# Performance work log

Hardware: AMD Instinct MI355X
Metric: run time of the kernel (lower is better)

The kernel has to match this reference:

```python
import jax, jax.numpy as jnp
import numpy as np
from jax.ops import segment_sum, segment_max

LRELU = 0.01  # torch F.leaky_relu default negative_slope


def _seg_softmax(e, seg, n):
    # torch_geometric.utils.softmax: stable segment softmax with 1e-16 eps
    m = segment_max(e, seg, num_segments=n)
    ex = jnp.exp(e - m[seg])
    s = segment_sum(ex, seg, num_segments=n)
    return ex / (s[seg] + 1e-16)


def _gcn(x, ei, w):
    j, i = ei[0], ei[1]  # code unpacks (edge_index_j, edge_index_i)
    n = x.shape[0]
    deg = segment_sum(jnp.ones_like(x[:, 0])[i], i, num_segments=n)
    dis = jnp.where(deg > 0, deg ** -0.5, 0.0)
    norm = dis[j] * dis[i]
    agg = segment_sum(norm[:, None] * x[j], i, num_segments=n)  # out[i] += norm*x[j]
    return jax.nn.relu(agg) @ w


def _highway(x1, x2, w, b):
    gate = jax.nn.sigmoid(x1 @ w + b)
    return gate * x2 + (1.0 - gate) * x1


def _gat_r(x, ei, a_i, a_j):
    j, i = ei[0], ei[1]
    n = x.shape[0]
    si = x @ a_i  # [R]
    sj = x @ a_j
    e = si[i] + sj[j]
    alpha = _seg_softmax(jax.nn.leaky_relu(e, LRELU).astype(jnp.float32), j, n)  # grouped by j!
    return jax.nn.relu(segment_sum(alpha[:, None] * x[j], i, num_segments=n))


def _graphattention_wjq(x, ei, rel_all, rel_emb, ww1):
    i, j = ei[0], ei[1]  # this module unpacks (i, j)
    n = x.shape[0]
    ef = jax.nn.leaky_relu(x, LRELU)
    re = jax.nn.leaky_relu(rel_emb, LRELU)
    feat = jnp.concatenate([ef[i], re[rel_all], ef[j]], axis=1)  # [E, 700]
    att = _seg_softmax(feat @ ww1, i, n)
    return segment_sum(feat * att[:, None], i, num_segments=n)  # [N, 700]


def _gat(x, r, ei, rel, a_i, a_j, a_r):
    j, i = ei[0], ei[1]
    n = x.shape[0]
    e = (x @ a_i)[i] + (x @ a_j)[j] + (r @ a_r)[rel]
    alpha = _seg_softmax(jax.nn.leaky_relu(e, LRELU).astype(jnp.float32), i, n)
    return jax.nn.relu(segment_sum(alpha[:, None] * x[j], i, num_segments=n))


def setup_inputs() -> dict:
    key = jax.random.key(0)
    ks = jax.random.split(key, 24)
    N, E, R, ELG, EH, RH = 20000, 150000, 1000, 15000, 300, 100

    def edges(k, n_nodes, n_edges):
        k1, k2 = jax.random.split(k)
        src = jax.random.randint(k1, (n_edges,), 0, n_nodes)
        dst = jax.random.randint(k2, (n_edges,), 0, n_nodes)
        src = jnp.where(src == dst, (src + 1) % n_nodes, src)  # no self-loops
        ring = jnp.arange(n_nodes)  # guarantee in-degree >= 1 everywhere
        src = src.at[:n_nodes].set((ring + 1) % n_nodes)
        dst = dst.at[:n_nodes].set(ring)
        return jnp.stack([src, dst])  # row0 = j (source), row1 = i (target)

    rel = jax.random.randint(ks[3], (E,), 0, R).at[0].set(R - 1)  # branch -> rel_emb1
    p = lambda k, sh: (jax.random.normal(k, sh, jnp.float32) * 0.05)
    return {
        "x_e": jax.random.normal(ks[0], (N, EH), jnp.float32),
        "edge_index": edges(ks[1], N, E),
        "rel": rel,
        "edge_index_all": edges(ks[2], N, E),
        "rel_all": jax.random.randint(ks[4], (E,), 0, 2 * R),
        "line_graph_index_out": edges(ks[5], R, ELG),
        "line_graph_val_out": jax.random.normal(ks[6], (ELG,), jnp.float32),
        "line_graph_index_in": edges(ks[7], R, ELG),
        "line_graph_val_in": jax.random.normal(ks[8], (ELG,), jnp.float32),
        "gcn1_w": p(ks[9], (EH, EH)),
        "gcn2_w": p(ks[10], (EH, EH)),
        "hw1_w": p(ks[11], (EH, EH)),
        "hw1_b": jnp.zeros((EH,), jnp.float32),
        "hw2_w": p(ks[12], (EH, EH)),
        "hw2_b": jnp.zeros((EH,), jnp.float32),
        "ww1": p(ks[13], (2 * EH + RH,)),
        "gat_ai": p(ks[14], (2 * (2 * EH + RH) - 400 + 0,)) if False else p(ks[14], (1000,)),
        "gat_aj": p(ks[15], (1000,)),
        "gat_ar": p(ks[16], (RH,)),
        "gatr_ai": p(ks[17], (RH,)),
        "gatr_aj": p(ks[18], (RH,)),
        "rel_emb1": p(ks[19], (R, RH)),
        "rel_emb2": p(ks[20], (R, RH)),
    }


def reference(x_e, edge_index, rel, edge_index_all, rel_all,
              line_graph_index_out, line_graph_val_out,
              line_graph_index_in, line_graph_val_in,
              gcn1_w, gcn2_w, hw1_w, hw1_b, hw2_w, hw2_b, ww1,
              gat_ai, gat_aj, gat_ar, gatr_ai, gatr_aj, rel_emb1, rel_emb2):
    # RAGA.forward; inputs constructed so rel.max()+1 == rel_emb1.shape[0]
    # (branch taken) and edge_index_all has no self-loops (remove_self_loops no-op).
    x = _highway(x_e, _gcn(x_e, edge_index_all, gcn1_w), hw1_w, hw1_b)
    x = _highway(x, _gcn(x, edge_index_all, gcn2_w), hw2_w, hw2_b)
    rel_emb_out = _gat_r(rel_emb1, line_graph_index_out, gatr_ai, gatr_aj)
    rel_emb_in = _gat_r(rel_emb1, line_graph_index_in, gatr_ai, gatr_aj)
    rel_emb = jnp.concatenate([rel_emb_out, rel_emb_in], axis=0)  # [2R, 100]
    x_wjq = jnp.concatenate(
        [x, _graphattention_wjq(x, edge_index_all, rel_all, rel_emb, ww1)], axis=1)  # [N, 1000]
    out = jnp.concatenate(
        [x_wjq, _gat(x_wjq, rel_emb, edge_index_all, rel_all, gat_ai, gat_aj, gat_ar)], axis=1)
    return out  # [N, 2000]
```

## Files before the change

### kernel.cpp

```cpp
#include <hip/hip_runtime.h>
#include <math.h>

#define LSL 0.01f

typedef _Float16 half8 __attribute__((ext_vector_type(8)));
typedef _Float16 half4 __attribute__((ext_vector_type(4)));
typedef float floatx4 __attribute__((ext_vector_type(4)));

static __device__ __forceinline__ float lrelu_f(float x){ return x > 0.f ? x : LSL * x; }
static __device__ __forceinline__ void atomAddF(float* p, float v){ unsafeAtomicAdd(p, v); }

__global__ void k_count2(const int* __restrict__ dstA, const int* __restrict__ srcA,
                         int* __restrict__ degD, int* __restrict__ degS, int E){
  int e = blockIdx.x * blockDim.x + threadIdx.x;
  if (e < E){ atomicAdd(degD + dstA[e], 1); atomicAdd(degS + srcA[e], 1); }
}

__global__ __launch_bounds__(1024)
void k_scan2(const int* __restrict__ cntD, int* __restrict__ offD,
             const int* __restrict__ cntS, int* __restrict__ offS, int n){
  const int* cnt = blockIdx.x ? cntS : cntD;
  int* off = blockIdx.x ? offS : offD;
  int t = threadIdx.x, lane = t & 63, wid = t >> 6;
  int len = (n + 1023) >> 10;
  int lo = t * len, hi = min(lo + len, n);
  int s = 0;
  for (int k = lo; k < hi; k++) s += cnt[k];
  int ws = s;
  #pragma unroll
  for (int o = 1; o < 64; o <<= 1){
    int u = __shfl_up(ws, o);
    if (lane >= o) ws += u;
  }
  __shared__ int wtot[16];
  if (lane == 63) wtot[wid] = ws;
  __syncthreads();
  int wpre = 0;
  #pragma unroll
  for (int k2 = 0; k2 < 16; k2++) wpre += (k2 < wid) ? wtot[k2] : 0;
  int run = wpre + ws - s;
  for (int k = lo; k < hi; k++){ off[k] = run; run += cnt[k]; }
  if (t == 0){
    int tot = 0;
    #pragma unroll
    for (int k2 = 0; k2 < 16; k2++) tot += wtot[k2];
    off[n] = tot;
  }
}

__global__ void k_fill_inv(const int* __restrict__ dstA, const int* __restrict__ srcA,
                           const int* __restrict__ offD, const int* __restrict__ offS,
                           int* __restrict__ curD, int* __restrict__ curS,
                           int* __restrict__ permD, int* __restrict__ permS,
                           const int* __restrict__ degD, float* __restrict__ dis,
                           int E, int N, int FB){
  int b = blockIdx.x, t = threadIdx.x;
  if (b < FB){
    int e = b * 256 + t;
    if (e >= E) return;
    int i = dstA[e];
    permD[offD[i] + atomicAdd(curD + i, 1)] = e;
    int j = srcA[e];
    permS[offS[j] + atomicAdd(curS + j, 1)] = e;
  } else {
    int v = (b - FB) * 256 + t;
    if (v < N){ int d = degD[v]; dis[v] = d > 0 ? rsqrtf((float)d) : 0.f; }
  }
}

__global__ __launch_bounds__(256)
void k_conv_f16(const float* __restrict__ x, _Float16* __restrict__ xh,
                float* __restrict__ sxi, float* __restrict__ sxj, int N){
  int i = blockIdx.x, t = threadIdx.x;
  _Float16* o = xh + (size_t)i * 320;
  if (i < N){
    const float* r = x + (size_t)i * 300;
    o[t] = (_Float16)r[t];
    if (t < 44) o[t + 256] = (_Float16)r[t + 256];
    else if (t < 64) o[t + 256] = (_Float16)0.f;
    if (t == 0) sxi[i] = 0.f;
    if (t == 1) sxj[i] = 0.f;
  } else {
    o[t] = (_Float16)0.f;
    if (t < 64) o[t + 256] = (_Float16)0.f;
  }
}

__global__ __launch_bounds__(256)
void k_gcn_gather(const int* __restrict__ off, const int* __restrict__ perm,
                  const int* __restrict__ src, const _Float16* __restrict__ x,
                  const float* __restrict__ dis, _Float16* __restrict__ agg, int N){
  int i = (int)(((long)blockIdx.x * blockDim.x + threadIdx.x) >> 6);
  int lane = threadIdx.x & 63;
  if (i >= N) return;
  int p0 = off[i], p1 = off[i+1];
  float di = dis[i];
  float acc[8] = {0.f,0.f,0.f,0.f,0.f,0.f,0.f,0.f};
  for (int base = p0; base < p1; base += 64){
    int m = min(64, p1 - base);
    int jj = 0; float wl = 0.f;
    if (base + lane < p1){
      int e = perm[base + lane];
      jj = src[e];
      wl = di * dis[jj];
    }
    int q = 0;
    for (; q + 1 < m; q += 2){
      int j0 = __shfl(jj, q),   j1 = __shfl(jj, q+1);
      float w0 = __shfl(wl, q), w1 = __shfl(wl, q+1);
      if (lane < 40){
        half8 v0 = *(const half8*)(x + (size_t)j0 * 320 + 8*lane);
        half8 v1 = *(const half8*)(x + (size_t)j1 * 320 + 8*lane);
        #pragma unroll
        for (int k = 0; k < 8; k++) acc[k] += w0 * (float)v0[k] + w1 * (float)v1[k];
      }
    }
    if (q < m){
      int j0 = __shfl(jj, q);
      float w0 = __shfl(wl, q);
      if (lane < 40){
        half8 v0 = *(const half8*)(x + (size_t)j0 * 320 + 8*lane);
        #pragma unroll
        for (int k = 0; k < 8; k++) acc[k] += w0 * (float)v0[k];
      }
    }
  }
  if (lane < 40){
    half8 o;
    #pragma unroll
    for (int k = 0; k < 8; k++) o[k] = (_Float16)fmaxf(acc[k], 0.f);
    *(half8*)(agg + (size_t)i * 320 + 8*lane) = o;
  }
}

__global__ void k_prep_B4(const float* __restrict__ W0, const float* __restrict__ W1,
                          const float* __restrict__ W2, const float* __restrict__ W3,
                          _Float16* __restrict__ BfAll){
  int idx = blockIdx.x * 256 + threadIdx.x;
  if (idx >= 4*12800) return;
  int wsel = idx / 12800;
  int rem2 = idx % 12800;
  const float* W = (wsel == 0) ? W0 : (wsel == 1) ? W1 : (wsel == 2) ? W2 : W3;
  int lane = rem2 & 63;
  int rem = rem2 >> 6;
  int nf = rem & 3; rem >>= 2;
  int nt = rem % 5;
  int ks = rem / 5;
  int n = nt*64 + nf*16 + (lane & 15);
  int kb = ks*32 + (lane >> 4) * 8;
  _Float16* o = BfAll + (size_t)wsel * 102400 + (size_t)rem2 * 8;
  #pragma unroll
  for (int e = 0; e < 8; e++){
    int k = kb + e;
    float v = (k < 300 && n < 300) ? W[(size_t)k * 300 + n] : 0.f;
    o[e] = (_Float16)v;
  }
}

__global__ __launch_bounds__(256)
void k_dual_mfma(const _Float16* __restrict__ A1, const _Float16* __restrict__ Xh,
                 const _Float16* __restrict__ Bf1, const _Float16* __restrict__ Bf2,
                 const float* __restrict__ bias, float* __restrict__ Of32, long ldo,
                 _Float16* __restrict__ Oh, long ldm, int M,
                 const float* __restrict__ ww, float* __restrict__ sxi,
                 float* __restrict__ sxj){
  int nb = gridDim.x;
  int q = nb >> 3, r = nb & 7;
  int xcd = blockIdx.x & 7, kk0 = blockIdx.x >> 3;
  int pseudo = (xcd < r ? xcd * (q + 1) : r * (q + 1) + (xcd - r) * q) + kk0;
  int nt = pseudo % 5;
  int panel = pseudo / 5;

  int tid = threadIdx.x;
  int w = tid >> 6, lane = tid & 63;
  int l15 = lane & 15, lg = lane >> 4;
  int rowBase = panel * 64 + w * 16;
  int colBase = nt * 64;

  floatx4 acc1[4], acc2[4];
  #pragma unroll
  for (int b = 0; b < 4; b++){
    acc1[b] = (floatx4){0.f,0.f,0.f,0.f};
    acc2[b] = (floatx4){0.f,0.f,0.f,0.f};
  }

  int row0 = rowBase + l15;
  const _Float16* a1p0 = A1 + (size_t)row0 * 320;
  const _Float16* a2p0 = Xh + (size_t)row0 * 320;

  for (int ks = 0; ks < 10; ks++){
    int kA = ks*32 + lg*8;
    half8 a1f0 = *(const half8*)(a1p0 + kA);
    half8 a2f0 = *(const half8*)(a2p0 + kA);
    const half8* b1p = (const half8*)Bf1 + ((size_t)(ks*5 + nt) * 4 * 64 + lane);
    const half8* b2p = (const half8*)Bf2 + ((size_t)(ks*5 + nt) * 4 * 64 + lane);
    #pragma unroll
    for (int nf = 0; nf < 4; nf++){
      half8 b1 = b1p[nf*64];
      half8 b2 = b2p[nf*64];
      acc1[nf] = __builtin_amdgcn_mfma_f32_16x16x32_f16(a1f0, b1, acc1[nf], 0,0,0);
      acc2[nf] = __builtin_amdgcn_mfma_f32_16x16x32_f16(a2f0, b2, acc2[nf], 0,0,0);
    }
  }

  bool doSX = (sxi != nullptr);
  float dA[4] = {0.f,0.f,0.f,0.f}, dB[4] = {0.f,0.f,0.f,0.f};
  #pragma unroll
  for (int nf = 0; nf < 4; nf++){
    int gn = colBase + nf*16 + l15;
    int gnc = min(gn, 299);
    float bv = bias[gnc];
    float wA = doSX ? ww[gnc] : 0.f;
    float wB = doSX ? ww[400 + gnc] : 0.f;
    #pragma unroll
    for (int r2 = 0; r2 < 4; r2++){
      int gm = rowBase + lg*4 + r2;
      int gmc = min(gm, M-1);
      float xv = (float)Xh[(size_t)gmc * 320 + gnc];
      float g = 1.f / (1.f + expf(-(acc2[nf][r2] + bv)));
      float val = g * acc1[nf][r2] + (1.f - g) * xv;
      if (gm < M && gn < 300){
        if (Of32) Of32[(size_t)gm * ldo + gn] = val;
        if (Oh)   Oh[(size_t)gm * ldm + gn] = (_Float16)val;
        float f = lrelu_f(val);
        dA[r2] += f * wA;
        dB[r2] += f * wB;
      }
    }
  }
  if (doSX){
    #pragma unroll
    for (int r2 = 0; r2 < 4; r2++){
      float a = dA[r2], b = dB[r2];
      #pragma unroll
      for (int o = 1; o < 16; o <<= 1){
        a += __shfl_xor(a, o);
        b += __shfl_xor(b, o);
      }
      int gm = rowBase + lg*4 + r2;
      if (l15 == 0 && gm < M){
        atomAddF(sxi + gm, a);
        atomAddF(sxj + gm, b);
      }
    }
  }
}

__global__ __launch_bounds__(256)
void k_wjq_gather(const int* __restrict__ off, const int* __restrict__ perm,
                  const int* __restrict__ dstA, const int* __restrict__ relI,
                  const float* __restrict__ sxi, const float* __restrict__ sxj,
                  const float* __restrict__ aRel, const _Float16* __restrict__ relEmbH,
                  const float* __restrict__ gat_ai, const float* __restrict__ gat_aj,
                  float* __restrict__ out, _Float16* __restrict__ xh2,
                  float* __restrict__ gxi, float* __restrict__ gxj,
                  float* __restrict__ sAl, int N){
  int i = (int)(((long)blockIdx.x * blockDim.x + threadIdx.x) >> 6);
  int lane = threadIdx.x & 63;
  if (i >= N) return;
  int p0 = off[i], p1 = off[i+1];
  int deg = p1 - p0;
  float si = sxi[i];
  float accx[8] = {0.f,0.f,0.f,0.f,0.f,0.f,0.f,0.f};
  float accr[4] = {0.f,0.f,0.f,0.f};
  float sumA;

  if (deg <= 64){
    int jj = 0, rr = 0; float l = -3.4e38f;
    if (lane < deg){
      int e = perm[p0 + lane];
      jj = dstA[e]; rr = relI[e];
      l = si + sxj[jj] + aRel[rr];
    }
    float lm = l;
    #pragma unroll
    for (int o = 32; o > 0; o >>= 1) lm = fmaxf(lm, __shfl_xor(lm, o));
    float exl = (lane < deg) ? expf(l - lm) : 0.f;
    float ls = exl;
    #pragma unroll
    for (int o = 32; o > 0; o >>= 1) ls += __shfl_xor(ls, o);
    float inv = 1.f / (ls + 1e-16f);
    sumA = ls * inv;
    float wgt = exl * inv;
    int qe = 0;
    for (; qe + 1 < deg; qe += 2){
      int j0 = __shfl(jj, qe),  j1 = __shfl(jj, qe+1);
      int r0 = __shfl(rr, qe),  r1 = __shfl(rr, qe+1);
      float a0 = __shfl(wgt, qe), a1 = __shfl(wgt, qe+1);
      if (lane < 38){
        half8 v0 = *(const half8*)(xh2 + (size_t)j0 * 1024 + 8*lane);
        half8 v1 = *(const half8*)(xh2 + (size_t)j1 * 1024 + 8*lane);
        #pragma unroll
        for (int k = 0; k < 8; k++)
          accx[k] += a0 * lrelu_f((float)v0[k]) + a1 * lrelu_f((float)v1[k]);
      } else if (lane < 63){
        half4 v0 = *(const half4*)(relEmbH + (size_t)r0 * 100 + 4*(lane - 38));
        half4 v1 = *(const half4*)(relEmbH + (size_t)r1 * 100 + 4*(lane - 38));
        #pragma unroll
        for (int k = 0; k < 4; k++)
          accr[k] += a0 * (float)v0[k] + a1 * (float)v1[k];
      }
    }
    if (qe < deg){
      int j0 = __shfl(jj, qe);
      int r0 = __shfl(rr, qe);
      float a0 = __shfl(wgt, qe);
      if (lane < 38){
        half8 v0 = *(const half8*)(xh2 + (size_t)j0 * 1024 + 8*lane);
        #pragma unroll
        for (int k = 0; k < 8; k++) accx[k] += a0 * lrelu_f((float)v0[k]);
      } else if (lane < 63){
        half4 v0 = *(const half4*)(relEmbH + (size_t)r0 * 100 + 4*(lane - 38));
        #pragma unroll
        for (int k = 0; k < 4; k++) accr[k] += a0 * (float)v0[k];
      }
    }
  } else {
    float lm = -3.4e38f;
    for (int p = p0 + lane; p < p1; p += 64){
      int e = perm[p];
      lm = fmaxf(lm, si + sxj[dstA[e]] + aRel[relI[e]]);
    }
    #pragma unroll
    for (int o = 32; o > 0; o >>= 1) lm = fmaxf(lm, __shfl_xor(lm, o));
    float ls = 0.f;
    for (int p = p0 + lane; p < p1; p += 64){
      int e = perm[p];
      ls += expf(si + sxj[dstA[e]] + aRel[relI[e]] - lm);
    }
    #pragma unroll
    for (int o = 32; o > 0; o >>= 1) ls += __shfl_xor(ls, o);
    float inv = 1.f / (ls + 1e-16f);
    sumA = ls * inv;
    for (int base = p0; base < p1; base += 64){
      int m = min(64, p1 - base);
      int jj = 0, rr = 0; float all = 0.f;
      if (base + lane < p1){
        int e = perm[base + lane];
        jj = dstA[e]; rr = relI[e];
        all = expf(si + sxj[jj] + aRel[rr] - lm) * inv;
      }
      for (int qe = 0; qe < m; qe++){
        int j = __shfl(jj, qe);
        int r = __shfl(rr, qe);
        float al = __shfl(all, qe);
        if (lane < 38){
          half8 v = *(const half8*)(xh2 + (size_t)j * 1024 + 8*lane);
          #pragma unroll
          for (int k = 0; k < 8; k++) accx[k] += al * lrelu_f((float)v[k]);
        } else if (lane < 63){
          half4 v = *(const half4*)(relEmbH + (size_t)r * 100 + 4*(lane - 38));
          #pragma unroll
          for (int k = 0; k < 4; k++) accr[k] += al * (float)v[k];
        }
      }
    }
  }

  float* oi = out + (size_t)i * 2000;
  _Float16* hi = xh2 + (size_t)i * 1024;
  float dA = 0.f, dB = 0.f;
  if (lane < 38){
    #pragma unroll
    for (int k = 0; k < 8; k++){
      int c = 8*lane + k;
      if (c < 300){
        oi[700 + c] = accx[k]; hi[700 + c] = (_Float16)accx[k];
        dA += accx[k] * gat_ai[700 + c];
        dB += accx[k] * gat_aj[700 + c];
      }
    }
    half8 v = *(const half8*)(hi + 8*lane);
    #pragma unroll
    for (int k = 0; k < 8; k++){
      int c = 8*lane + k;
      if (c < 300){
        float x2v = (float)v[k];
        float h = lrelu_f(x2v) * sumA;
        oi[300 + c] = h;
        dA += x2v * gat_ai[c] + h * gat_ai[300 + c];
        dB += x2v * gat_aj[c] + h * gat_aj[300 + c];
      }
    }
  } else if (lane < 63){
    #pragma unroll
    for (int k = 0; k < 4; k++){
      int c = 4*(lane - 38) + k;
      oi[600 + c] = accr[k]; hi[600 + c] = (_Float16)accr[k];
      dA += accr[k] * gat_ai[600 + c];
      dB += accr[k] * gat_aj[600 + c];
    }
  }
  #pragma unroll
  for (int o = 32; o > 0; o >>= 1){
    dA += __shfl_xor(dA, o);
    dB += __shfl_xor(dB, o);
  }
  if (lane == 0){ gxi[i] = dA; gxj[i] = dB; sAl[i] = sumA; }
}

__global__ __launch_bounds__(256)
void k_gat_gather(const int* __restrict__ off, const int* __restrict__ perm,
                  const int* __restrict__ srcA, const int* __restrict__ relI,
                  const float* __restrict__ gxi, const float* __restrict__ gxj,
                  const float* __restrict__ srr, const float* __restrict__ sAl,
                  const _Float16* __restrict__ xh2, float* __restrict__ out, int N){
  long gw = ((long)blockIdx.x * blockDim.x + threadIdx.x) >> 6;
  int lane = threadIdx.x & 63;
  int i = (int)(gw >> 1), half = (int)(gw & 1);
  if (i >= N) return;
  int p0 = off[i], p1 = off[i+1];
  int deg = p1 - p0;
  float gi = gxi[i];
  float acc_a[8] = {0.f,0.f,0.f,0.f,0.f,0.f,0.f,0.f};
  float acc_b[8] = {0.f,0.f,0.f,0.f,0.f,0.f,0.f,0.f};

  if (deg <= 64){
    int jj = 0; float l = -3.4e38f, saj = 0.f;
    if (lane < deg){
      int e = perm[p0 + lane];
      jj = srcA[e];
      l = lrelu_f(gi + gxj[jj] + srr[relI[e]]);
      if (half == 0) saj = sAl[jj];
    }
    float lm = l;
    #pragma unroll
    for (int o = 32; o > 0; o >>= 1) lm = fmaxf(lm, __shfl_xor(lm, o));
    float exl = (lane < deg) ? expf(l - lm) : 0.f;
    float ls = exl;
    #pragma unroll
    for (int o = 32; o > 0; o >>= 1) ls += __shfl_xor(ls, o);
    float wgt = exl / (ls + 1e-16f);
    if (half == 0){
      int qe = 0;
      for (; qe + 1 < deg; qe += 2){
        int j0 = __shfl(jj, qe),    j1 = __shfl(jj, qe+1);
        float a0 = __shfl(wgt, qe), a1 = __shfl(wgt, qe+1);
        float s0 = __shfl(saj, qe) * a0, s1 = __shfl(saj, qe+1) * a1;
        if (lane < 38){
          half8 v0 = *(const half8*)(xh2 + (size_t)j0 * 1024 + 8*lane);
          half8 v1 = *(const half8*)(xh2 + (size_t)j1 * 1024 + 8*lane);
          #pragma unroll
          for (int k = 0; k < 8; k++){
            float x0 = (float)v0[k], x1 = (float)v1[k];
            acc_a[k] += a0 * x0 + a1 * x1;
            acc_b[k] += s0 * lrelu_f(x0) + s1 * lrelu_f(x1);
          }
        }
      }
      if (qe < deg){
        int j0 = __shfl(jj, qe);
        float a0 = __shfl(wgt, qe);
        float s0 = __shfl(saj, qe) * a0;
        if (lane < 38){
          half8 v0 = *(const half8*)(xh2 + (size_t)j0 * 1024 + 8*lane);
          #pragma unroll
          for (int k = 0; k < 8; k++){
            float x0 = (float)v0[k];
            acc_a[k] += a0 * x0;
            acc_b[k] += s0 * lrelu_f(x0);
          }
        }
      }
    } else {
      int qe = 0;
      for (; qe + 1 < deg; qe += 2){
        int j0 = __shfl(jj, qe),    j1 = __shfl(jj, qe+1);
        float a0 = __shfl(wgt, qe), a1 = __shfl(wgt, qe+1);
        if (lane < 50){
          half8 v0 = *(const half8*)(xh2 + (size_t)j0 * 1024 + 600 + 8*lane);
          half8 v1 = *(const half8*)(xh2 + (size_t)j1 * 1024 + 600 + 8*lane);
          #pragma unroll
          for (int k = 0; k < 8; k++) acc_a[k] += a0 * (float)v0[k] + a1 * (float)v1[k];
        }
      }
      if (qe < deg){
        int j0 = __shfl(jj, qe);
        float a0 = __shfl(wgt, qe);
        if (lane < 50){
          half8 v0 = *(const half8*)(xh2 + (size_t)j0 * 1024 + 600 + 8*lane);
          #pragma unroll
          for (int k = 0; k < 8; k++) acc_a[k] += a0 * (float)v0[k];
        }
      }
    }
  } else {
    float lm = -3.4e38f;
    for (int p = p0 + lane; p < p1; p += 64){
      int e = perm[p];
      lm = fmaxf(lm, lrelu_f(gi + gxj[srcA[e]] + srr[relI[e]]));
    }
    #pragma unroll
    for (int o = 32; o > 0; o >>= 1) lm = fmaxf(lm, __shfl_xor(lm, o));
    float ls = 0.f;
    for (int p = p0 + lane; p < p1; p += 64){
      int e = perm[p];
      ls += expf(lrelu_f(gi + gxj[srcA[e]] + srr[relI[e]]) - lm);
    }
    #pragma unroll
    for (int o = 32; o > 0; o >>= 1) ls += __shfl_xor(ls, o);
    float inv = 1.f / (ls + 1e-16f);
    for (int base = p0; base < p1; base += 64){
      int m = min(64, p1 - base);
      int jj = 0; float all = 0.f, saj = 0.f;
      if (base + lane < p1){
        int e = perm[base + lane];
        jj = srcA[e];
        all = expf(lrelu_f(gi + gxj[jj] + srr[relI[e]]) - lm) * inv;
        if (half == 0) saj = sAl[jj];
      }
      for (int qe = 0; qe < m; qe++){
        int j = __shfl(jj, qe);
        float al = __shfl(all, qe);
        if (half == 0){
          float sa = __shfl(saj, qe) * al;
          if (lane < 38){
            half8 v = *(const half8*)(xh2 + (size_t)j * 1024 + 8*lane);
            #pragma unroll
            for (int k = 0; k < 8; k++){
              float x0 = (float)v[k];
              acc_a[k] += al * x0;
              acc_b[k] += sa * lrelu_f(x0);
            }
          }
        } else {
          if (lane < 50){
            half8 v = *(const half8*)(xh2 + (size_t)j * 1024 + 600 + 8*lane);
            #pragma unroll
            for (int k = 0; k < 8; k++) acc_a[k] += al * (float)v[k];
          }
        }
      }
    }
  }

  float* ob = out + (size_t)i * 2000 + 1000;
  if (half == 0){
    if (lane < 37){
      floatx4 s0, s1, t0, t1;
      #pragma unroll
      for (int k = 0; k < 4; k++){
        s0[k] = fmaxf(acc_a[k], 0.f);   s1[k] = fmaxf(acc_a[4+k], 0.f);
        t0[k] = fmaxf(acc_b[k], 0.f);   t1[k] = fmaxf(acc_b[4+k], 0.f);
      }
      *(floatx4*)(ob + 8*lane) = s0;
      *(floatx4*)(ob + 8*lane + 4) = s1;
      *(floatx4*)(ob + 300 + 8*lane) = t0;
      *(floatx4*)(ob + 300 + 8*lane + 4) = t1;
    } else if (lane == 37){
      #pragma unroll
      for (int k = 0; k < 4; k++){
        ob[296 + k] = fmaxf(acc_a[k], 0.f);
        ob[596 + k] = fmaxf(acc_b[k], 0.f);
      }
    }
  } else {
    if (lane < 50){
      floatx4 s0, s1;
      #pragma unroll
      for (int k = 0; k < 4; k++){ s0[k] = fmaxf(acc_a[k], 0.f); s1[k] = fmaxf(acc_a[4+k], 0.f); }
      *(floatx4*)(ob + 600 + 8*lane) = s0;
      *(floatx4*)(ob + 600 + 8*lane + 4) = s1;
    }
  }
}

__global__ void k_dot2_small(const float* __restrict__ X, int ld, int len,
                             const float* __restrict__ wA, const float* __restrict__ wB,
                             float* __restrict__ oA, float* __restrict__ oB,
                             int n, int applyL){
  int v = blockIdx.x * blockDim.x + threadIdx.x;
  if (v >= n) return;
  const float* row = X + (size_t)v * ld;
  float a = 0.f, b = 0.f;
  for (int c = 0; c < len; c++){
    float f = row[c];
    if (applyL) f = lrelu_f(f);
    a += f * wA[c];
    if (wB) b += f * wB[c];
  }
  oA[v] = a;
  if (oB) oB[v] = b;
}

__global__ void k_relu_dots(float* __restrict__ relEmb, _Float16* __restrict__ relEmbH,
                            const float* __restrict__ wA, const float* __restrict__ wB,
                            float* __restrict__ aRel, float* __restrict__ srr, int n){
  int v = blockIdx.x * blockDim.x + threadIdx.x;
  if (v >= n) return;
  float* row = relEmb + (size_t)v * 100;
  _Float16* rowH = relEmbH + (size_t)v * 100;
  float a = 0.f, b = 0.f;
  for (int c = 0; c < 100; c++){
    float f = fmaxf(row[c], 0.f);
    row[c] = f;
    rowH[c] = (_Float16)f;
    a += f * wA[c];
    b += f * wB[c];
  }
  aRel[v] = a;
  srr[v] = b;
}

__global__ void k_lg_le(const int* __restrict__ lgOut, const int* __restrict__ lgIn,
                        int ELG, int R, const float* __restrict__ sR_i,
                        const float* __restrict__ sR_j,
                        float* __restrict__ elog, float* __restrict__ sumR){
  int e = blockIdx.x * blockDim.x + threadIdx.x;
  if (e >= 2*ELG) return;
  int g = e >= ELG;
  int el = e - g*ELG;
  const int* lg = g ? lgIn : lgOut;
  int j = lg[el], i = lg[el + ELG];
  float ex = expf(lrelu_f(sR_j[j] + sR_i[i]));
  elog[e] = ex;
  atomAddF(sumR + g*R + j, ex);
}

__global__ void k_lg_scatter(const int* __restrict__ lgOut, const int* __restrict__ lgIn,
                             int ELG, int R, const float* __restrict__ ex,
                             const float* __restrict__ sumR,
                             const float* __restrict__ relEmb1, float* __restrict__ relEmb){
  int e = blockIdx.x;
  int g = e >= ELG;
  int el = e - g*ELG;
  const int* lg = g ? lgIn : lgOut;
  int j = lg[el], i = lg[el + ELG];
  float alpha = ex[e] / (sumR[g*R + j] + 1e-16f);
  const float* xj = relEmb1 + (size_t)j * 100;
  float* oi = relEmb + (size_t)(g*R + i) * 100;
  for (int c = threadIdx.x; c < 100; c += blockDim.x)
    atomAddF(oi + c, alpha * xj[c]);
}

extern "C" void kernel_launch(void* const* d_in, const int* in_sizes, int n_in,
                              void* d_out, int out_size, void* d_ws, size_t ws_size,
                              hipStream_t stream){
  const float* x_e     = (const float*)d_in[0];
  const int*   eiA     = (const int*)  d_in[3];
  const int*   relAll  = (const int*)  d_in[4];
  const int*   lgOut   = (const int*)  d_in[5];
  const int*   lgIn    = (const int*)  d_in[7];
  const float* gcn1_w  = (const float*)d_in[9];
  const float* gcn2_w  = (const float*)d_in[10];
  const float* hw1_w   = (const float*)d_in[11];
  const float* hw1_b   = (const float*)d_in[12];
  const float* hw2_w   = (const float*)d_in[13];
  const float* hw2_b   = (const float*)d_in[14];
  const float* ww1     = (const float*)d_in[15];
  const float* gat_ai  = (const float*)d_in[16];
  const float* gat_aj  = (const float*)d_in[17];
  const float* gat_ar  = (const float*)d_in[18];
  const float* gatr_ai = (const float*)d_in[19];
  const float* gatr_aj = (const float*)d_in[20];
  const float* relEmb1 = (const float*)d_in[21];

  const int EH = 300, RH = 100;
  const int N   = in_sizes[0] / EH;
  const int E   = in_sizes[3] / 2;
  const int ELG = in_sizes[5] / 2;
  const int R   = in_sizes[21] / RH;
  const int Mtiles = (N + 127) / 128;
  const int Mpad = Mtiles * 128;

  char* base = (char*)d_ws;
  _Float16* xh0   = (_Float16*)base;  base += (size_t)Mpad * 320 * 2;
  _Float16* xhA   = (_Float16*)base;  base += (size_t)Mpad * 320 * 2;
  _Float16* A1f16 = (_Float16*)base;  base += (size_t)Mpad * 320 * 2;
  _Float16* xh2   = (_Float16*)base;  base += (size_t)N * 1024 * 2;
  _Float16* BfAll = (_Float16*)base;  base += (size_t)4 * 102400 * 2;
  _Float16* relEmbH = (_Float16*)base; base += (size_t)2 * R * RH * 2;
  float* w = (float*)base;
  float* dis    = w; w += N;
  float* relEmb = w; w += (size_t)2 * R * RH;
  float* sumR   = w; w += 2 * R;
  float* sxi    = w; w += N;
  float* sxj    = w; w += N;
  float* gxi    = w; w += N;
  float* gxj    = w; w += N;
  float* sAl    = w; w += N;
  float* sR_i   = w; w += R;
  float* sR_j   = w; w += R;
  float* aRel   = w; w += 2 * R;
  float* srr    = w; w += 2 * R;
  float* eE     = w; w += E;
  int* degD   = (int*)w; w += N;
  int* degS   = (int*)w; w += N;
  int* curD   = (int*)w; w += N;
  int* curS   = (int*)w; w += N;
  int* offD   = (int*)w; w += N + 1;
  int* offS   = (int*)w; w += N + 1;
  int* permD  = (int*)w; w += E;
  int* permS  = (int*)w; w += E;

  _Float16* Bf_g1 = BfAll;
  _Float16* Bf_h1 = BfAll + 102400;
  _Float16* Bf_g2 = BfAll + 2 * 102400;
  _Float16* Bf_h2 = BfAll + 3 * 102400;

  float* out = (float*)d_out;
  const int* srcA = eiA;
  const int* dstA = eiA + E;

  auto cdiv = [](int a, int b){ return (a + b - 1) / b; };

  hipMemsetAsync(degD, 0, (size_t)4 * N * 4, stream);
  k_count2<<<cdiv(E,256),256,0,stream>>>(dstA, srcA, degD, degS, E);
  k_scan2<<<2,1024,0,stream>>>(degD, offD, degS, offS, N);
  int FB = cdiv(E,256);
  k_fill_inv<<<FB + cdiv(N,256),256,0,stream>>>(dstA, srcA, offD, offS, curD, curS,
                                                permD, permS, degD, dis, E, N, FB);

  k_prep_B4<<<200,256,0,stream>>>(gcn1_w, hw1_w, gcn2_w, hw2_w, BfAll);
  k_conv_f16<<<Mpad,256,0,stream>>>(x_e, xh0, sxi, sxj, N);

  int NB = 5 * (Mpad / 64);
  int GW = cdiv(N, 4);

  k_gcn_gather<<<GW,256,0,stream>>>(offD, permD, srcA, xh0, dis, A1f16, N);
  k_dual_mfma<<<NB,256,0,stream>>>(A1f16, xh0, Bf_g1, Bf_h1, hw1_b,
                                   nullptr, 0, xhA, 320, N, nullptr, nullptr, nullptr);

  k_gcn_gather<<<GW,256,0,stream>>>(offD, permD, srcA, xhA, dis, A1f16, N);
  k_dual_mfma<<<NB,256,0,stream>>>(A1f16, xhA, Bf_g2, Bf_h2, hw2_b,
                                   out, 2000, xh2, 1024, N, ww1, sxi, sxj);

  k_dot2_small<<<cdiv(R,256),256,0,stream>>>(relEmb1, RH, RH, gatr_ai, gatr_aj, sR_i, sR_j, R, 0);
  hipMemsetAsync(relEmb, 0, ((size_t)2*R*RH + 2*R) * 4, stream);
  k_lg_le<<<cdiv(2*ELG,256),256,0,stream>>>(lgOut, lgIn, ELG, R, sR_i, sR_j, eE, sumR);
  k_lg_scatter<<<2*ELG,128,0,stream>>>(lgOut, lgIn, ELG, R, eE, sumR, relEmb1, relEmb);

  k_relu_dots<<<cdiv(2*R,256),256,0,stream>>>(relEmb, relEmbH, ww1 + EH, gat_ar, aRel, srr, 2*R);

  k_wjq_gather<<<GW,256,0,stream>>>(offS, permS, dstA, relAll, sxi, sxj, aRel, relEmbH,
                                    gat_ai, gat_aj, out, xh2, gxi, gxj, sAl, N);

  k_gat_gather<<<cdiv(N,2),256,0,stream>>>(offD, permD, srcA, relAll, gxi, gxj, srr,
                                           sAl, xh2, out, N);
}
```

Before: 392.4 us.

## Fuse setup kernels into one launch and split GAT gather into three column parts

Four independent setup kernels (degree counting, weight repacking to fp16 MFMA layout, x conversion to fp16, relation score dots) are merged into one block-partitioned launch to cut launch overhead. The GAT gather now gives each node three wavefronts instead of two: one for columns 0-303 plus the alpha-weighted extra, and two covering 600-799 and 800-999. This balances the per-wave column work and raises parallelism, at the cost of recomputing the per-node softmax in one more wave.

```diff
diff --git a/kernel.cpp b/kernel.cpp
--- a/kernel.cpp
+++ b/kernel.cpp
@@ -10,10 +10,68 @@
 static __device__ __forceinline__ float lrelu_f(float x){ return x > 0.f ? x : LSL * x; }
 static __device__ __forceinline__ void atomAddF(float* p, float v){ unsafeAtomicAdd(p, v); }
 
-__global__ void k_count2(const int* __restrict__ dstA, const int* __restrict__ srcA,
-                         int* __restrict__ degD, int* __restrict__ degS, int E){
-  int e = blockIdx.x * blockDim.x + threadIdx.x;
-  if (e < E){ atomicAdd(degD + dstA[e], 1); atomicAdd(degS + srcA[e], 1); }
+__global__ __launch_bounds__(256)
+void k_setup(const int* __restrict__ dstA, const int* __restrict__ srcA,
+             int* __restrict__ degD, int* __restrict__ degS, int E,
+             const float* __restrict__ W0, const float* __restrict__ W1,
+             const float* __restrict__ W2, const float* __restrict__ W3,
+             _Float16* __restrict__ BfAll,
+             const float* __restrict__ x_e, _Float16* __restrict__ xh0,
+             float* __restrict__ sxi, float* __restrict__ sxj, int N,
+             const float* __restrict__ relEmb1, const float* __restrict__ gatr_ai,
+             const float* __restrict__ gatr_aj, float* __restrict__ sR_i,
+             float* __restrict__ sR_j, int R, int B0, int B1, int B2){
+  int b = blockIdx.x, t = threadIdx.x;
+  if (b < B0){
+    int e = b * 256 + t;
+    if (e < E){ atomicAdd(degD + dstA[e], 1); atomicAdd(degS + srcA[e], 1); }
+  } else if (b < B0 + B1){
+    int idx = (b - B0) * 256 + t;
+    if (idx >= 4*12800) return;
+    int wsel = idx / 12800;
+    int rem2 = idx % 12800;
+    const float* W = (wsel == 0) ? W0 : (wsel == 1) ? W1 : (wsel == 2) ? W2 : W3;
+    int lane = rem2 & 63;
+    int rem = rem2 >> 6;
+    int nf = rem & 3; rem >>= 2;
+    int nt = rem % 5;
+    int ks = rem / 5;
+    int n = nt*64 + nf*16 + (lane & 15);
+    int kb = ks*32 + (lane >> 4) * 8;
+    _Float16* o = BfAll + (size_t)wsel * 102400 + (size_t)rem2 * 8;
+    #pragma unroll
+    for (int e = 0; e < 8; e++){
+      int k = kb + e;
+      float v = (k < 300 && n < 300) ? W[(size_t)k * 300 + n] : 0.f;
+      o[e] = (_Float16)v;
+    }
+  } else if (b < B0 + B1 + B2){
+    int i = b - B0 - B1;
+    _Float16* o = xh0 + (size_t)i * 320;
+    if (i < N){
+      const float* r = x_e + (size_t)i * 300;
+      o[t] = (_Float16)r[t];
+      if (t < 44) o[t + 256] = (_Float16)r[t + 256];
+      else if (t < 64) o[t + 256] = (_Float16)0.f;
+      if (t == 0) sxi[i] = 0.f;
+      if (t == 1) sxj[i] = 0.f;
+    } else {
+      o[t] = (_Float16)0.f;
+      if (t < 64) o[t + 256] = (_Float16)0.f;
+    }
+  } else {
+    int v = (b - B0 - B1 - B2) * 256 + t;
+    if (v >= R) return;
+    const float* row = relEmb1 + (size_t)v * 100;
+    float a = 0.f, c = 0.f;
+    for (int k = 0; k < 100; k++){
+      float f = row[k];
+      a += f * gatr_ai[k];
+      c += f * gatr_aj[k];
+    }
+    sR_i[v] = a;
+    sR_j[v] = c;
+  }
 }
 
 __global__ __launch_bounds__(1024)
@@ -69,24 +127,6 @@
 }
 
 __global__ __launch_bounds__(256)
-void k_conv_f16(const float* __restrict__ x, _Float16* __restrict__ xh,
-                float* __restrict__ sxi, float* __restrict__ sxj, int N){
-  int i = blockIdx.x, t = threadIdx.x;
-  _Float16* o = xh + (size_t)i * 320;
-  if (i < N){
-    const float* r = x + (size_t)i * 300;
-    o[t] = (_Float16)r[t];
-    if (t < 44) o[t + 256] = (_Float16)r[t + 256];
-    else if (t < 64) o[t + 256] = (_Float16)0.f;
-    if (t == 0) sxi[i] = 0.f;
-    if (t == 1) sxj[i] = 0.f;
-  } else {
-    o[t] = (_Float16)0.f;
-    if (t < 64) o[t + 256] = (_Float16)0.f;
-  }
-}
-
-__global__ __launch_bounds__(256)
 void k_gcn_gather(const int* __restrict__ off, const int* __restrict__ perm,
                   const int* __restrict__ src, const _Float16* __restrict__ x,
                   const float* __restrict__ dis, _Float16* __restrict__ agg, int N){
@@ -130,30 +170,6 @@
     #pragma unroll
     for (int k = 0; k < 8; k++) o[k] = (_Float16)fmaxf(acc[k], 0.f);
     *(half8*)(agg + (size_t)i * 320 + 8*lane) = o;
-  }
-}
-
-__global__ void k_prep_B4(const float* __restrict__ W0, const float* __restrict__ W1,
-                          const float* __restrict__ W2, const float* __restrict__ W3,
-                          _Float16* __restrict__ BfAll){
-  int idx = blockIdx.x * 256 + threadIdx.x;
-  if (idx >= 4*12800) return;
-  int wsel = idx / 12800;
-  int rem2 = idx % 12800;
-  const float* W = (wsel == 0) ? W0 : (wsel == 1) ? W1 : (wsel == 2) ? W2 : W3;
-  int lane = rem2 & 63;
-  int rem = rem2 >> 6;
-  int nf = rem & 3; rem >>= 2;
-  int nt = rem % 5;
-  int ks = rem / 5;
-  int n = nt*64 + nf*16 + (lane & 15);
-  int kb = ks*32 + (lane >> 4) * 8;
-  _Float16* o = BfAll + (size_t)wsel * 102400 + (size_t)rem2 * 8;
-  #pragma unroll
-  for (int e = 0; e < 8; e++){
-    int k = kb + e;
-    float v = (k < 300 && n < 300) ? W[(size_t)k * 300 + n] : 0.f;
-    o[e] = (_Float16)v;
   }
 }
 
@@ -407,11 +423,14 @@
                   const _Float16* __restrict__ xh2, float* __restrict__ out, int N){
   long gw = ((long)blockIdx.x * blockDim.x + threadIdx.x) >> 6;
   int lane = threadIdx.x & 63;
-  int i = (int)(gw >> 1), half = (int)(gw & 1);
+  int i = (int)(gw / 3), part = (int)(gw % 3);
   if (i >= N) return;
   int p0 = off[i], p1 = off[i+1];
   int deg = p1 - p0;
   float gi = gxi[i];
+  int cbase = (part == 0) ? 0 : (400 + part * 200);
+  int c0 = cbase + 8*lane;
+  bool act = (part == 0) ? (lane < 38) : (lane < 25);
   float acc_a[8] = {0.f,0.f,0.f,0.f,0.f,0.f,0.f,0.f};
   float acc_b[8] = {0.f,0.f,0.f,0.f,0.f,0.f,0.f,0.f};
 
@@ -421,7 +440,7 @@
       int e = perm[p0 + lane];
       jj = srcA[e];
       l = lrelu_f(gi + gxj[jj] + srr[relI[e]]);
-      if (half == 0) saj = sAl[jj];
+      if (part == 0) saj = sAl[jj];
     }
     float lm = l;
     #pragma unroll
@@ -431,13 +450,13 @@
     #pragma unroll
     for (int o = 32; o > 0; o >>= 1) ls += __shfl_xor(ls, o);
     float wgt = exl / (ls + 1e-16f);
-    if (half == 0){
+    if (part == 0){
       int qe = 0;
       for (; qe + 1 < deg; qe += 2){
         int j0 = __shfl(jj, qe),    j1 = __shfl(jj, qe+1);
         float a0 = __shfl(wgt, qe), a1 = __shfl(wgt, qe+1);
         float s0 = __shfl(saj, qe) * a0, s1 = __shfl(saj, qe+1) * a1;
-        if (lane < 38){
+        if (act){
           half8 v0 = *(const half8*)(xh2 + (size_t)j0 * 1024 + 8*lane);
           half8 v1 = *(const half8*)(xh2 + (size_t)j1 * 1024 + 8*lane);
           #pragma unroll
@@ -452,7 +471,7 @@
         int j0 = __shfl(jj, qe);
         float a0 = __shfl(wgt, qe);
         float s0 = __shfl(saj, qe) * a0;
-        if (lane < 38){
+        if (act){
           half8 v0 = *(const half8*)(xh2 + (size_t)j0 * 1024 + 8*lane);
           #pragma unroll
           for (int k = 0; k < 8; k++){
@@ -467,9 +486,9 @@
       for (; qe + 1 < deg; qe += 2){
         int j0 = __shfl(jj, qe),    j1 = __shfl(jj, qe+1);
         float a0 = __shfl(wgt, qe), a1 = __shfl(wgt, qe+1);
-        if (lane < 50){
-          half8 v0 = *(const half8*)(xh2 + (size_t)j0 * 1024 + 600 + 8*lane);
-          half8 v1 = *(const half8*)(xh2 + (size_t)j1 * 1024 + 600 + 8*lane);
+        if (act){
+          half8 v0 = *(const half8*)(xh2 + (size_t)j0 * 1024 + c0);
+          half8 v1 = *(const half8*)(xh2 + (size_t)j1 * 1024 + c0);
           #pragma unroll
           for (int k = 0; k < 8; k++) acc_a[k] += a0 * (float)v0[k] + a1 * (float)v1[k];
         }
@@ -477,8 +496,8 @@
       if (qe < deg){
         int j0 = __shfl(jj, qe);
         float a0 = __shfl(wgt, qe);
-        if (lane < 50){
-          half8 v0 = *(const half8*)(xh2 + (size_t)j0 * 1024 + 600 + 8*lane);
+        if (act){
+          half8 v0 = *(const half8*)(xh2 + (size_t)j0 * 1024 + c0);
           #pragma unroll
           for (int k = 0; k < 8; k++) acc_a[k] += a0 * (float)v0[k];
         }
@@ -507,14 +526,14 @@
         int e = perm[base + lane];
         jj = srcA[e];
         all = expf(lrelu_f(gi + gxj[jj] + srr[relI[e]]) - lm) * inv;
-        if (half == 0) saj = sAl[jj];
+        if (part == 0) saj = sAl[jj];
       }
       for (int qe = 0; qe < m; qe++){
         int j = __shfl(jj, qe);
         float al = __shfl(all, qe);
-        if (half == 0){
+        if (part == 0){
           float sa = __shfl(saj, qe) * al;
-          if (lane < 38){
+          if (act){
             half8 v = *(const half8*)(xh2 + (size_t)j * 1024 + 8*lane);
             #pragma unroll
             for (int k = 0; k < 8; k++){
@@ -524,8 +543,8 @@
             }
           }
         } else {
-          if (lane < 50){
-            half8 v = *(const half8*)(xh2 + (size_t)j * 1024 + 600 + 8*lane);
+          if (act){
+            half8 v = *(const half8*)(xh2 + (size_t)j * 1024 + c0);
             #pragma unroll
             for (int k = 0; k < 8; k++) acc_a[k] += al * (float)v[k];
           }
@@ -535,7 +554,7 @@
   }
 
   float* ob = out + (size_t)i * 2000 + 1000;
-  if (half == 0){
+  if (part == 0){
     if (lane < 37){
       floatx4 s0, s1, t0, t1;
       #pragma unroll
@@ -555,32 +574,14 @@
       }
     }
   } else {
-    if (lane < 50){
+    if (lane < 25){
       floatx4 s0, s1;
       #pragma unroll
       for (int k = 0; k < 4; k++){ s0[k] = fmaxf(acc_a[k], 0.f); s1[k] = fmaxf(acc_a[4+k], 0.f); }
-      *(floatx4*)(ob + 600 + 8*lane) = s0;
-      *(floatx4*)(ob + 600 + 8*lane + 4) = s1;
-    }
-  }
-}
-
-__global__ void k_dot2_small(const float* __restrict__ X, int ld, int len,
-                             const float* __restrict__ wA, const float* __restrict__ wB,
-                             float* __restrict__ oA, float* __restrict__ oB,
-                             int n, int applyL){
-  int v = blockIdx.x * blockDim.x + threadIdx.x;
-  if (v >= n) return;
-  const float* row = X + (size_t)v * ld;
-  float a = 0.f, b = 0.f;
-  for (int c = 0; c < len; c++){
-    float f = row[c];
-    if (applyL) f = lrelu_f(f);
-    a += f * wA[c];
-    if (wB) b += f * wB[c];
-  }
-  oA[v] = a;
-  if (oB) oB[v] = b;
+      *(floatx4*)(ob + c0) = s0;
+      *(floatx4*)(ob + c0 + 4) = s1;
+    }
+  }
 }
 
 __global__ void k_relu_dots(float* __restrict__ relEmb, _Float16* __restrict__ relEmbH,
@@ -705,15 +706,17 @@
   auto cdiv = [](int a, int b){ return (a + b - 1) / b; };
 
   hipMemsetAsync(degD, 0, (size_t)4 * N * 4, stream);
-  k_count2<<<cdiv(E,256),256,0,stream>>>(dstA, srcA, degD, degS, E);
+  int B0 = cdiv(E,256), B1 = 200, B2 = Mpad, B3 = cdiv(R,256);
+  k_setup<<<B0+B1+B2+B3,256,0,stream>>>(dstA, srcA, degD, degS, E,
+                                        gcn1_w, hw1_w, gcn2_w, hw2_w, BfAll,
+                                        x_e, xh0, sxi, sxj, N,
+                                        relEmb1, gatr_ai, gatr_aj, sR_i, sR_j, R,
+                                        B0, B1, B2);
   k_scan2<<<2,1024,0,stream>>>(degD, offD, degS, offS, N);
   int FB = cdiv(E,256);
   k_fill_inv<<<FB + cdiv(N,256),256,0,stream>>>(dstA, srcA, offD, offS, curD, curS,
                                                 permD, permS, degD, dis, E, N, FB);
 
-  k_prep_B4<<<200,256,0,stream>>>(gcn1_w, hw1_w, gcn2_w, hw2_w, BfAll);
-  k_conv_f16<<<Mpad,256,0,stream>>>(x_e, xh0, sxi, sxj, N);
-
   int NB = 5 * (Mpad / 64);
   int GW = cdiv(N, 4);
 
@@ -725,7 +728,6 @@
   k_dual_mfma<<<NB,256,0,stream>>>(A1f16, xhA, Bf_g2, Bf_h2, hw2_b,
                                    out, 2000, xh2, 1024, N, ww1, sxi, sxj);
 
-  k_dot2_small<<<cdiv(R,256),256,0,stream>>>(relEmb1, RH, RH, gatr_ai, gatr_aj, sR_i, sR_j, R, 0);
   hipMemsetAsync(relEmb, 0, ((size_t)2*R*RH + 2*R) * 4, stream);
   k_lg_le<<<cdiv(2*ELG,256),256,0,stream>>>(lgOut, lgIn, ELG, R, sR_i, sR_j, eE, sumR);
   k_lg_scatter<<<2*ELG,128,0,stream>>>(lgOut, lgIn, ELG, R, eE, sumR, relEmb1, relEmb);
@@ -735,6 +737,6 @@
   k_wjq_gather<<<GW,256,0,stream>>>(offS, permS, dstA, relAll, sxi, sxj, aRel, relEmbH,
                                     gat_ai, gat_aj, out, xh2, gxi, gxj, sAl, N);
 
-  k_gat_gather<<<cdiv(N,2),256,0,stream>>>(offD, permD, srcA, relAll, gxi, gxj, srr,
-                                           sAl, xh2, out, N);
-}
+  k_gat_gather<<<cdiv(3*N,4),256,0,stream>>>(offD, permD, srcA, relAll, gxi, gxj, srr,
+                                             sAl, xh2, out, N);
+}
```

New measurement: 373.6 us. 1.05x faster.
